# Kernel optimization log

Measured on AMD Instinct MI355X. Metric: run time of the kernel, lower is better.

## Reference

```python
import jax, jax.numpy as jnp
import numpy as np

B, C, H, W = 16, 1024, 32, 32
M = 32

def setup_inputs() -> dict:
    key = jax.random.key(0)
    k1, k2 = jax.random.split(key)
    features = jax.random.normal(k1, (B, C, H, W), dtype=jnp.float32)
    raw_attentions = jax.random.normal(k2, (B, M, H, W), dtype=jnp.float32)
    return {"features": features, "raw_attentions": raw_attentions}

def reference(features, raw_attentions):
    # non_lin='sigmoid'
    attentions = jax.nn.sigmoid(raw_attentions)  # [B, M, H, W]
    # GAP pooling of features * attentions[:, i] for each map i, fused as one
    # contraction: feature_matrix[b, m, c] = mean_{h,w} features[b,c,h,w] * att[b,m,h,w]
    hw = features.shape[2] * features.shape[3]
    feature_matrix = jnp.einsum('bchw,bmhw->bmc', features, attentions) / hw  # [B, M, C]
    return feature_matrix, attentions
```

## Files before the change

kernel.cpp:

```cpp
#include <hip/hip_runtime.h>
#include <cstdint>
#include <cstddef>


#define BB 16
#define CC 1024
#define MM 32
#define HW 1024

#define TKF 128
#define NSTF (HW / TKF)
#define TCR 64

typedef __attribute__((ext_vector_type(4))) float f32x4;
typedef __attribute__((ext_vector_type(8))) float f32x8;
typedef __attribute__((ext_vector_type(8))) short s16x8;

__device__ inline short bf16rne(float x)
{
    uint32_t u = __builtin_bit_cast(uint32_t, x);
    u = (u + 0x7FFFu + ((u >> 16) & 1u)) >> 16;
    return (short)u;
}

__device__ inline s16x8 cvt8(f32x4 lo, f32x4 hi)
{
    s16x8 r;
#pragma unroll
    for (int j = 0; j < 4; ++j) {
        r[j]     = bf16rne(lo[j]);
        r[4 + j] = bf16rne(hi[j]);
    }
    return r;
}

__device__ inline void gld_lds16(const void* g, void* l)
{
    __builtin_amdgcn_global_load_lds(
        (const __attribute__((address_space(1))) void*)g,
        (__attribute__((address_space(3))) void*)l, 16, 0, 0);
}

__global__ __launch_bounds__(256) void sigmoid_kernel(
    const float* __restrict__ raw, float* __restrict__ out1,
    unsigned short* __restrict__ ws)
{
    int g = blockIdx.x * 256 + threadIdx.x;
    f32x8 v = reinterpret_cast<const f32x8*>(raw)[g];
    f32x8 s;
    s16x8 h;
#pragma unroll
    for (int j = 0; j < 8; ++j) {
        s[j] = 1.0f / (1.0f + __expf(-v[j]));
        h[j] = bf16rne(s[j]);
    }
    reinterpret_cast<f32x8*>(out1)[g] = s;
    int b = g >> 12, row = (g >> 7) & 31, chunk = g & 127;
    int idx = (b << 12) + (row << 7) + (chunk ^ (row & 15));
    reinterpret_cast<s16x8*>(ws)[idx] = h;
}

__global__ __launch_bounds__(512) void bap_mfma(
    const float* __restrict__ feat,
    const unsigned short* __restrict__ ws,
    float* __restrict__ out0)
{
    __shared__ float fsh[2][TCR][TKF];
    __shared__ unsigned short att_lds[MM][HW];

    const int t  = threadIdx.x;
    const int w  = t >> 6;
    const int l  = t & 63;
    const int b  = blockIdx.x & 15;
    const int cg = blockIdx.x >> 4;
    const int cbase = cg * TCR;

    const int lrow  = l >> 5;
    const int lslot = l & 31;

    const float* fbase = feat + (size_t)(b * CC + cbase) * HW;
    const unsigned short* abase = ws + (size_t)b * MM * HW;

#pragma unroll
    for (int i = 0; i < 8; ++i) {
        int off16 = (w * 8 + i) * 64;
        gld_lds16(abase + (size_t)off16 * 8 + (size_t)l * 8,
                  &att_lds[0][0] + (size_t)off16 * 8);
    }

    auto stage = [&](int s, int nb) {
        const int k0 = s * TKF;
#pragma unroll
        for (int i = 0; i < 4; ++i) {
            int r0  = w * 8 + i * 2;
            int row = r0 + lrow;
            int sg  = lslot ^ (row & 15);
            gld_lds16(fbase + (size_t)row * HW + k0 + sg * 4,
                      &fsh[nb][r0][0]);
        }
    };

    const int r  = l & 15;
    const int q  = l >> 4;
    const int mt = w >> 2;
    const int c4 = w & 3;
    const int arow = mt * 16 + r;
    const int brow = c4 * 16 + r;
    const unsigned short* att_row = &att_lds[arow][0];

    f32x4 acc = {0.f, 0.f, 0.f, 0.f};

    auto compute = [&](int s, int nb) {
#pragma unroll
        for (int ch = 0; ch < 4; ++ch) {
            int aidx = ((s << 4) + (ch << 2) + q) ^ r;
            s16x8 af = *reinterpret_cast<const s16x8*>(att_row + aidx * 8);
            int S0 = (ch << 3) + (q << 1);
            f32x4 blo = *reinterpret_cast<const f32x4*>(
                &fsh[nb][brow][((S0 ^ r)) << 2]);
            f32x4 bhi = *reinterpret_cast<const f32x4*>(
                &fsh[nb][brow][(((S0 + 1) ^ r)) << 2]);
            acc = __builtin_amdgcn_mfma_f32_16x16x32_bf16(
                      af, cvt8(blo, bhi), acc, 0, 0, 0);
        }
    };

    stage(0, 0);
    __syncthreads();
#pragma unroll
    for (int s = 0; s < NSTF; ++s) {
        if (s + 1 < NSTF) stage(s + 1, (s + 1) & 1);
        compute(s, s & 1);
        __syncthreads();
    }

    const float sc = 1.0f / (float)HW;
    float* p = out0 + (size_t)(b * MM) * CC + cbase + c4 * 16;
#pragma unroll
    for (int reg = 0; reg < 4; ++reg)
        p[(size_t)(mt * 16 + 4 * q + reg) * CC + r] = acc[reg] * sc;
}

extern "C" void kernel_launch(void* const* d_in, const int* in_sizes, int n_in,
                              void* d_out, int out_size, void* d_ws, size_t ws_size,
                              hipStream_t stream)
{
    const float* feat = (const float*)d_in[0];
    const float* raw  = (const float*)d_in[1];
    float* out0 = (float*)d_out;
    float* out1 = out0 + (size_t)BB * MM * HW;
    unsigned short* att_bf = (unsigned short*)d_ws;

    sigmoid_kernel<<<256, 256, 0, stream>>>(raw, out1, att_bf);
    bap_mfma<<<256, 512, 0, stream>>>(feat, att_bf, out0);
}
```

Measured before the change: 22.90 us.

## Load attention operand directly to registers and halve channel tile

Removes the shared-memory staging of the full bf16 attention tile and instead loads the A operand for each K-stage directly from global memory into double-buffered registers; the workspace swizzle is dropped accordingly. The channel tile shrinks to 32 rows with 256-thread blocks, doubling the grid to 512 blocks and cutting LDS per block. This aims to improve occupancy and remove the large upfront LDS fill, at the cost of doubled attention reads from global/L2 and exposed global latency on the A path.

Measured after the change: 22.65 us, median of 2. Within noise of the previous version (-1.1%).

```diff
diff --git a/kernel.cpp b/kernel.cpp
--- a/kernel.cpp
+++ b/kernel.cpp
@@ -8,9 +8,9 @@
 #define MM 32
 #define HW 1024
 
+#define TCR 32
 #define TKF 128
 #define NSTF (HW / TKF)
-#define TCR 64
 
 typedef __attribute__((ext_vector_type(4))) float f32x4;
 typedef __attribute__((ext_vector_type(8))) float f32x8;
@@ -55,38 +55,27 @@
         h[j] = bf16rne(s[j]);
     }
     reinterpret_cast<f32x8*>(out1)[g] = s;
-    int b = g >> 12, row = (g >> 7) & 31, chunk = g & 127;
-    int idx = (b << 12) + (row << 7) + (chunk ^ (row & 15));
-    reinterpret_cast<s16x8*>(ws)[idx] = h;
+    reinterpret_cast<s16x8*>(ws)[g] = h;
 }
 
-__global__ __launch_bounds__(512) void bap_mfma(
+__global__ __launch_bounds__(256) void bap_mfma(
     const float* __restrict__ feat,
     const unsigned short* __restrict__ ws,
     float* __restrict__ out0)
 {
     __shared__ float fsh[2][TCR][TKF];
-    __shared__ unsigned short att_lds[MM][HW];
 
     const int t  = threadIdx.x;
     const int w  = t >> 6;
     const int l  = t & 63;
     const int b  = blockIdx.x & 15;
-    const int cg = blockIdx.x >> 4;
-    const int cbase = cg * TCR;
+    const int ct = blockIdx.x >> 4;
+    const int cbase = ct * TCR;
 
     const int lrow  = l >> 5;
     const int lslot = l & 31;
 
     const float* fbase = feat + (size_t)(b * CC + cbase) * HW;
-    const unsigned short* abase = ws + (size_t)b * MM * HW;
-
-#pragma unroll
-    for (int i = 0; i < 8; ++i) {
-        int off16 = (w * 8 + i) * 64;
-        gld_lds16(abase + (size_t)off16 * 8 + (size_t)l * 8,
-                  &att_lds[0][0] + (size_t)off16 * 8);
-    }
 
     auto stage = [&](int s, int nb) {
         const int k0 = s * TKF;
@@ -102,40 +91,50 @@
 
     const int r  = l & 15;
     const int q  = l >> 4;
-    const int mt = w >> 2;
-    const int c4 = w & 3;
+    const int mt = w >> 1;
+    const int c2 = w & 1;
     const int arow = mt * 16 + r;
-    const int brow = c4 * 16 + r;
-    const unsigned short* att_row = &att_lds[arow][0];
+    const int brow = c2 * 16 + r;
+    const s16x8* ap = reinterpret_cast<const s16x8*>(
+        ws + (size_t)(b * MM + arow) * HW);
+
+    s16x8 af[2][4];
+    auto load_af = [&](int s, int pb) {
+#pragma unroll
+        for (int ch = 0; ch < 4; ++ch)
+            af[pb][ch] = ap[s * 16 + ch * 4 + q];
+    };
 
     f32x4 acc = {0.f, 0.f, 0.f, 0.f};
 
-    auto compute = [&](int s, int nb) {
+    auto compute = [&](int s, int nb, int pb) {
 #pragma unroll
         for (int ch = 0; ch < 4; ++ch) {
-            int aidx = ((s << 4) + (ch << 2) + q) ^ r;
-            s16x8 af = *reinterpret_cast<const s16x8*>(att_row + aidx * 8);
-            int S0 = (ch << 3) + (q << 1);
+            const int S0 = ch * 8 + 2 * q;
             f32x4 blo = *reinterpret_cast<const f32x4*>(
-                &fsh[nb][brow][((S0 ^ r)) << 2]);
+                &fsh[nb][brow][(S0 ^ r) * 4]);
             f32x4 bhi = *reinterpret_cast<const f32x4*>(
-                &fsh[nb][brow][(((S0 + 1) ^ r)) << 2]);
+                &fsh[nb][brow][((S0 + 1) ^ r) * 4]);
             acc = __builtin_amdgcn_mfma_f32_16x16x32_bf16(
-                      af, cvt8(blo, bhi), acc, 0, 0, 0);
+                      af[pb][ch], cvt8(blo, bhi), acc, 0, 0, 0);
         }
     };
 
+    load_af(0, 0);
     stage(0, 0);
     __syncthreads();
 #pragma unroll
     for (int s = 0; s < NSTF; ++s) {
-        if (s + 1 < NSTF) stage(s + 1, (s + 1) & 1);
-        compute(s, s & 1);
+        if (s + 1 < NSTF) {
+            load_af(s + 1, (s + 1) & 1);
+            stage(s + 1, (s + 1) & 1);
+        }
+        compute(s, s & 1, s & 1);
         __syncthreads();
     }
 
     const float sc = 1.0f / (float)HW;
-    float* p = out0 + (size_t)(b * MM) * CC + cbase + c4 * 16;
+    float* p = out0 + (size_t)(b * MM) * CC + cbase + c2 * 16;
 #pragma unroll
     for (int reg = 0; reg < 4; ++reg)
         p[(size_t)(mt * 16 + 4 * q + reg) * CC + r] = acc[reg] * sc;
@@ -152,5 +151,5 @@
     unsigned short* att_bf = (unsigned short*)d_ws;
 
     sigmoid_kernel<<<256, 256, 0, stream>>>(raw, out1, att_bf);
-    bap_mfma<<<256, 512, 0, stream>>>(feat, att_bf, out0);
+    bap_mfma<<<512, 256, 0, stream>>>(feat, att_bf, out0);
 }
```
